# Kernel tuning notes

Hardware: AMD Instinct MI355X
Metric: run time of the kernel (lower is better)

## Reference

```python
import jax, jax.numpy as jnp
import numpy as np
import math

B, S, CIN, H, W = 8, 8, 64, 32, 32
COUT, K = 128, 3
PW = COUT * CIN * K * K  # 73728
P = PW + COUT            # 73856


def setup_inputs() -> dict:
    key = jax.random.key(0)
    ks = jax.random.split(key, 6)
    return {
        "x": jax.random.normal(ks[0], (B, S, CIN, H, W), dtype=jnp.float32),
        "e": jax.random.normal(ks[1], (S, P), dtype=jnp.float32),
        "mu_w": jax.random.normal(ks[2], (PW,), dtype=jnp.float32) * 0.02,
        "rho_w": jax.random.normal(ks[3], (PW,), dtype=jnp.float32) * 0.5,
        "mu_b": jax.random.normal(ks[4], (COUT,), dtype=jnp.float32) * 0.02,
        "rho_b": jax.random.normal(ks[5], (COUT,), dtype=jnp.float32) * 0.5,
    }


def _unit_log_mfg(v):
    # v: [s_n, D]; -log(2*pi)*D/2 - sum(v**2)/2  (scalar, matching torch code)
    two_pi = jnp.asarray(2.0 * math.pi, v.dtype)
    return -jnp.log(two_pi) * (v.shape[1] / 2.0) - jnp.sum(v * v) / 2.0


def reference(x, e, mu_w, rho_w, mu_b, rho_b):
    s_n = e.shape[0]
    cout = mu_b.shape[0]
    cin = x.shape[2]
    k = int(round(math.sqrt(mu_w.shape[0] / (cout * cin))))
    pw = mu_w.shape[0]

    sig_w = jax.nn.softplus(rho_w)  # log(1+exp(rho))
    sig_b = jax.nn.softplus(rho_b)
    w = mu_w[None, :] + sig_w[None, :] * e[:, :pw]          # [s_n, PW]
    b = mu_b[None, :] + sig_b[None, :] * e[:, pw:pw + cout]  # [s_n, COUT]

    entropy_q = jnp.sum(jnp.log(sig_w)) + jnp.sum(jnp.log(sig_b))
    cross_entropy_qp = _unit_log_mfg(w) + _unit_log_mfg(b)
    kl_qp = -entropy_q - cross_entropy_qp

    w5 = w.reshape(s_n, cout, cin, k, k)  # per-sample OIHW kernels

    # per-sample conv: vmap over the sample axis j; batch conv over data axis i
    def conv_one(xj, wj):  # xj [B,CIN,H,W], wj [COUT,CIN,K,K]
        return jax.lax.conv(xj, wj, (1, 1), 'VALID')

    out = jax.vmap(conv_one, in_axes=(1, 0), out_axes=1)(x, w5)  # [B,S,COUT,H',W']
    out = out + b[None, :, :, None, None]
    return out, kl_qp
```

## Files before the change

### kernel.cpp

```cpp
#include <hip/hip_runtime.h>
#include <hip/hip_bf16.h>
#include <math.h>

#define Bn    8
#define Sn    8
#define COUTc 128
#define PWc   73728
#define Pc    73856
#define WOc   30
#define NPIX  900
#define GPIX  7200
#define NSTEP 9
#define TILE  128
#define NT2   57

typedef __bf16 bf16;
typedef bf16  bf16x8 __attribute__((ext_vector_type(8)));
typedef float f32x16 __attribute__((ext_vector_type(16)));

__device__ __forceinline__ float softplus_f(float x) {
    return fmaxf(x, 0.f) + log1pf(expf(-fabsf(x)));
}

__device__ __forceinline__ unsigned int pack2(float a, float b) {
    unsigned short ua = __builtin_bit_cast(unsigned short, (bf16)a);
    unsigned short ub = __builtin_bit_cast(unsigned short, (bf16)b);
    return ((unsigned int)ub << 16) | (unsigned int)ua;
}

__device__ __forceinline__ void gl16(const void* g, void* l) {
    typedef __attribute__((address_space(1))) void gvoid;
    typedef __attribute__((address_space(3))) void lvoid;
    __builtin_amdgcn_global_load_lds((gvoid*)g, (lvoid*)l, 16, 0, 0);
}

__global__ __launch_bounds__(256) void prep_all(
        const float* __restrict__ xg, const float* __restrict__ e,
        const float* __restrict__ mu_w, const float* __restrict__ rho_w,
        const float* __restrict__ mu_b, const float* __restrict__ rho_b,
        bf16* __restrict__ xt, bf16* __restrict__ wimg,
        float* __restrict__ bq, float* __restrict__ slots) {
    const int bid = blockIdx.x;
    const int t   = threadIdx.x;

    if (bid < 512) {
        const int img  = bid >> 3;
        const int part = bid & 7;
        const int p    = part * 128 + (t >> 1);
        const int half = t & 1;
        const float* src = xg + ((size_t)img << 16) + (size_t)(half * 32) * 1024 + p;
        bf16*        dst = xt + ((size_t)img << 16) + (size_t)p * 64 + half * 32;
        #pragma unroll
        for (int o = 0; o < 4; ++o) {
            uint4 pk;
            pk.x = pack2(src[(o * 8 + 0) * 1024], src[(o * 8 + 1) * 1024]);
            pk.y = pack2(src[(o * 8 + 2) * 1024], src[(o * 8 + 3) * 1024]);
            pk.z = pack2(src[(o * 8 + 4) * 1024], src[(o * 8 + 5) * 1024]);
            pk.w = pack2(src[(o * 8 + 6) * 1024], src[(o * 8 + 7) * 1024]);
            *reinterpret_cast<uint4*>(dst + o * 8) = pk;
        }
        return;
    }

    float ls = 0.f, sq = 0.f;
    if (bid < 800) {
        const int rb    = bid - 512;
        const int r     = rb >> 5;
        const int chunk = rb & 31;
        const int idx   = chunk * 256 + t;
        const int co    = idx >> 6;
        const int ci    = idx & 63;
        const int p     = co * 576 + ci * 9 + r;
        float sig = softplus_f(rho_w[p]);
        ls = logf(sig);
        float mu = mu_w[p];
        const int dstp = (co << 6) + (((ci >> 3) ^ (co & 7)) << 3) + (ci & 7);
        #pragma unroll
        for (int s = 0; s < Sn; ++s) {
            float wv = fmaf(sig, e[s * Pc + p], mu);
            wimg[((s * NSTEP + r) << 13) + dstp] = (bf16)wv;
            sq += wv * wv;
        }
    } else {
        if (t < COUTc) {
            float sig = softplus_f(rho_b[t]);
            ls = logf(sig);
            float mu = mu_b[t];
            #pragma unroll
            for (int s = 0; s < Sn; ++s) {
                float bv = fmaf(sig, e[s * Pc + PWc + t], mu);
                bq[s * COUTc + t] = bv;
                sq += bv * bv;
            }
        }
    }

    #pragma unroll
    for (int off = 32; off > 0; off >>= 1) {
        ls += __shfl_down(ls, off);
        sq += __shfl_down(sq, off);
    }
    __shared__ float sls[4], ssq[4];
    const int lane = t & 63, wd = t >> 6;
    if (lane == 0) { sls[wd] = ls; ssq[wd] = sq; }
    __syncthreads();
    if (t == 0) {
        slots[2 * (bid - 512)]     = sls[0] + sls[1] + sls[2] + sls[3];
        slots[2 * (bid - 512) + 1] = ssq[0] + ssq[1] + ssq[2] + ssq[3];
    }
}

__global__ __launch_bounds__(256) void conv_mfma(
        const bf16* __restrict__ xt, const bf16* __restrict__ wimg,
        const float* __restrict__ bq, const float* __restrict__ slots,
        float* __restrict__ out, float* __restrict__ klout) {
    const int bid  = blockIdx.x;
    const int s    = bid & 7;
    const int tile = bid >> 3;
    const int t    = threadIdx.x;
    const int lane = t & 63;
    const int w    = t >> 6;
    const int wr   = w >> 1;
    const int wc   = w & 1;

    __shared__ bf16 Wbuf[2][8192];
    __shared__ bf16 Xbuf[2][8192];

    const char* wsrcL = (const char*)wimg + ((size_t)(s * NSTEP) << 14)
                      + (w << 12) + (lane << 4);

    const char *x0, *x1, *x2, *x3;
    #pragma unroll
    for (int q = 0; q < 4; ++q) {
        int pix = w * 32 + q * 8 + (lane >> 3);
        int g   = tile * TILE + pix;
        if (g >= GPIX) g = GPIX - 1;
        int b2 = g / NPIX;
        int rr = g - b2 * NPIX;
        int oy = rr / WOc;
        int ox = rr - oy * WOc;
        int m  = (lane & 7) ^ (pix & 7);
        const char* ptr = (const char*)xt
            + ((((size_t)(b2 * Sn + s) << 10) + oy * 32 + ox) << 7) + (m << 4);
        if (q == 0) x0 = ptr; else if (q == 1) x1 = ptr;
        else if (q == 2) x2 = ptr; else x3 = ptr;
    }

    f32x16 acc[2][2];
    #pragma unroll
    for (int i = 0; i < 2; ++i)
        #pragma unroll
        for (int j = 0; j < 2; ++j)
            #pragma unroll
            for (int k = 0; k < 16; ++k)
                acc[i][j][k] = 0.f;

    #define STAGE(stepc, b)                                                  \
    {                                                                        \
        const char* ws_ = wsrcL + ((stepc) << 14);                           \
        char* wl_ = (char*)(&Wbuf[(b)][0]) + (w << 12);                      \
        gl16(ws_,        wl_);                                               \
        gl16(ws_ + 1024, wl_ + 1024);                                        \
        gl16(ws_ + 2048, wl_ + 2048);                                        \
        gl16(ws_ + 3072, wl_ + 3072);                                        \
        const int roff_ = (((stepc) / 3) * 32 + ((stepc) % 3)) * 128;        \
        char* xl_ = (char*)(&Xbuf[(b)][0]) + (w << 12);                      \
        gl16(x0 + roff_, xl_);                                               \
        gl16(x1 + roff_, xl_ + 1024);                                        \
        gl16(x2 + roff_, xl_ + 2048);                                        \
        gl16(x3 + roff_, xl_ + 3072);                                        \
    }

    #define COMPUTE(b)                                                       \
    {                                                                        \
        const bf16* Wl_ = &Wbuf[(b)][0];                                     \
        const bf16* Xl_ = &Xbuf[(b)][0];                                     \
        _Pragma("unroll")                                                    \
        for (int kc = 0; kc < 4; ++kc) {                                     \
            const int oct_ = ((kc << 1) + (lane >> 5)) ^ (lane & 7);         \
            bf16x8 af0 = *reinterpret_cast<const bf16x8*>(                   \
                Wl_ + ((wr * 64 + (lane & 31)) << 6) + (oct_ << 3));         \
            bf16x8 af1 = *reinterpret_cast<const bf16x8*>(                   \
                Wl_ + ((wr * 64 + 32 + (lane & 31)) << 6) + (oct_ << 3));    \
            bf16x8 bf0 = *reinterpret_cast<const bf16x8*>(                   \
                Xl_ + ((wc * 64 + (lane & 31)) << 6) + (oct_ << 3));         \
            bf16x8 bf1 = *reinterpret_cast<const bf16x8*>(                   \
                Xl_ + ((wc * 64 + 32 + (lane & 31)) << 6) + (oct_ << 3));    \
            acc[0][0] = __builtin_amdgcn_mfma_f32_32x32x16_bf16(af0, bf0, acc[0][0], 0, 0, 0); \
            acc[0][1] = __builtin_amdgcn_mfma_f32_32x32x16_bf16(af0, bf1, acc[0][1], 0, 0, 0); \
            acc[1][0] = __builtin_amdgcn_mfma_f32_32x32x16_bf16(af1, bf0, acc[1][0], 0, 0, 0); \
            acc[1][1] = __builtin_amdgcn_mfma_f32_32x32x16_bf16(af1, bf1, acc[1][1], 0, 0, 0); \
        }                                                                    \
    }

    STAGE(0, 0);
    STAGE(1, 1);

    #define ITER(tt, b)                                                      \
        asm volatile("s_waitcnt vmcnt(8)" ::: "memory");                     \
        __builtin_amdgcn_s_barrier();                                        \
        __builtin_amdgcn_sched_barrier(0);                                   \
        COMPUTE(b);                                                          \
        __builtin_amdgcn_sched_barrier(0);                                   \
        __builtin_amdgcn_s_barrier();                                        \
        STAGE((tt) + 2, b);

    ITER(0, 0)
    ITER(1, 1)
    ITER(2, 0)
    ITER(3, 1)
    ITER(4, 0)
    ITER(5, 1)
    ITER(6, 0)
    asm volatile("s_waitcnt vmcnt(8)" ::: "memory");
    __builtin_amdgcn_s_barrier();
    __builtin_amdgcn_sched_barrier(0);
    COMPUTE(1);
    asm volatile("s_waitcnt vmcnt(0)" ::: "memory");
    __builtin_amdgcn_s_barrier();
    __builtin_amdgcn_sched_barrier(0);
    COMPUTE(0);

    #undef ITER
    #undef COMPUTE
    #undef STAGE

    const int colp = lane & 31;
    const int hi   = lane >> 5;
    #pragma unroll
    for (int ti = 0; ti < 2; ++ti) {
        float bs[16];
        #pragma unroll
        for (int reg = 0; reg < 16; ++reg) {
            int co = wr * 64 + ti * 32 + (reg & 3) + 8 * (reg >> 2) + 4 * hi;
            bs[reg] = bq[s * COUTc + co];
        }
        #pragma unroll
        for (int tj = 0; tj < 2; ++tj) {
            int gg = tile * TILE + wc * 64 + tj * 32 + colp;
            if (gg >= GPIX) continue;
            int b2 = gg / NPIX;
            int r2 = gg - b2 * NPIX;
            float* ob = out + (size_t)(b2 * Sn + s) * (COUTc * NPIX) + r2;
            #pragma unroll
            for (int reg = 0; reg < 16; ++reg) {
                int co = wr * 64 + ti * 32 + (reg & 3) + 8 * (reg >> 2) + 4 * hi;
                ob[co * NPIX] = acc[ti][tj][reg] + bs[reg];
            }
        }
    }

    if (bid == 0 && w == 0) {
        float ls = 0.f, sq = 0.f;
        for (int i = lane; i < 289; i += 64) {
            ls += slots[2 * i];
            sq += slots[2 * i + 1];
        }
        #pragma unroll
        for (int off = 32; off > 0; off >>= 1) {
            ls += __shfl_down(ls, off);
            sq += __shfl_down(sq, off);
        }
        if (lane == 0)
            *klout = -ls + 0.91893853320467274f * (float)Pc + 0.5f * sq;
    }
}

extern "C" void kernel_launch(void* const* d_in, const int* in_sizes, int n_in,
                              void* d_out, int out_size, void* d_ws, size_t ws_size,
                              hipStream_t stream) {
    const float* x     = (const float*)d_in[0];
    const float* e     = (const float*)d_in[1];
    const float* mu_w  = (const float*)d_in[2];
    const float* rho_w = (const float*)d_in[3];
    const float* mu_b  = (const float*)d_in[4];
    const float* rho_b = (const float*)d_in[5];
    float* out = (float*)d_out;

    bf16*  wimg  = (bf16*)d_ws;
    float* bq    = (float*)((char*)d_ws + 1179648);
    float* slots = (float*)((char*)d_ws + 1183744);
    bf16*  xt    = (bf16*)((char*)d_ws + 1187840);

    prep_all<<<dim3(801), dim3(256), 0, stream>>>(
        x, e, mu_w, rho_w, mu_b, rho_b, xt, wimg, bq, slots);

    conv_mfma<<<dim3(NT2 * Sn), dim3(256), 0, stream>>>(
        xt, wimg, bq, slots, out, out + (out_size - 1));
}
```

Before: 30.23 us.

## Vectorize prep loads, merge weight-tap blocks, restructure conv pipeline

The x transpose now reads float4 vectors per channel octet and writes four pixel rows per thread. Weight prep handles all nine taps per thread, so the launch shrinks from 801 to 545 blocks and each block reads e contiguously. The conv main loop changes from a 2-deep prefetch with vmcnt(8) to a one-stage-ahead pattern that waits for vmcnt(0) every iteration, which may expose more load latency. The KL slot reduction shrinks to a serial 33-entry loop on one thread.

```diff
diff --git a/kernel.cpp b/kernel.cpp
--- a/kernel.cpp
+++ b/kernel.cpp
@@ -16,6 +16,7 @@
 
 typedef __bf16 bf16;
 typedef bf16  bf16x8 __attribute__((ext_vector_type(8)));
+typedef float f32x4v __attribute__((ext_vector_type(4)));
 typedef float f32x16 __attribute__((ext_vector_type(16)));
 
 __device__ __forceinline__ float softplus_f(float x) {
@@ -44,42 +45,50 @@
     const int t   = threadIdx.x;
 
     if (bid < 512) {
-        const int img  = bid >> 3;
-        const int part = bid & 7;
-        const int p    = part * 128 + (t >> 1);
-        const int half = t & 1;
-        const float* src = xg + ((size_t)img << 16) + (size_t)(half * 32) * 1024 + p;
-        bf16*        dst = xt + ((size_t)img << 16) + (size_t)p * 64 + half * 32;
-        #pragma unroll
-        for (int o = 0; o < 4; ++o) {
+        const int img = bid >> 3;
+        const int oct = t & 7;
+        const int p0  = ((bid & 7) * 32 + (t >> 3)) * 4;
+        const float* src = xg + ((size_t)img << 16) + (size_t)(oct * 8) * 1024 + p0;
+        f32x4v v[8];
+        #pragma unroll
+        for (int j = 0; j < 8; ++j)
+            v[j] = *reinterpret_cast<const f32x4v*>(src + (size_t)j * 1024);
+        char* dstB = (char*)xt + (((size_t)(img << 10) + p0) << 7) + (oct << 4);
+        #pragma unroll
+        for (int i = 0; i < 4; ++i) {
             uint4 pk;
-            pk.x = pack2(src[(o * 8 + 0) * 1024], src[(o * 8 + 1) * 1024]);
-            pk.y = pack2(src[(o * 8 + 2) * 1024], src[(o * 8 + 3) * 1024]);
-            pk.z = pack2(src[(o * 8 + 4) * 1024], src[(o * 8 + 5) * 1024]);
-            pk.w = pack2(src[(o * 8 + 6) * 1024], src[(o * 8 + 7) * 1024]);
-            *reinterpret_cast<uint4*>(dst + o * 8) = pk;
+            pk.x = pack2(v[0][i], v[1][i]);
+            pk.y = pack2(v[2][i], v[3][i]);
+            pk.z = pack2(v[4][i], v[5][i]);
+            pk.w = pack2(v[6][i], v[7][i]);
+            *reinterpret_cast<uint4*>(dstB + (size_t)i * 128) = pk;
         }
         return;
     }
 
     float ls = 0.f, sq = 0.f;
-    if (bid < 800) {
-        const int rb    = bid - 512;
-        const int r     = rb >> 5;
-        const int chunk = rb & 31;
-        const int idx   = chunk * 256 + t;
-        const int co    = idx >> 6;
-        const int ci    = idx & 63;
-        const int p     = co * 576 + ci * 9 + r;
-        float sig = softplus_f(rho_w[p]);
-        ls = logf(sig);
-        float mu = mu_w[p];
+    if (bid < 544) {
+        const int gidx = (bid - 512) * 256 + t;
+        const int co   = gidx >> 6;
+        const int ci   = gidx & 63;
+        const int p0   = co * 576 + ci * 9;
+        float mu[9], sg[9];
+        #pragma unroll
+        for (int r = 0; r < 9; ++r) {
+            mu[r] = mu_w[p0 + r];
+            sg[r] = softplus_f(rho_w[p0 + r]);
+            ls   += logf(sg[r]);
+        }
         const int dstp = (co << 6) + (((ci >> 3) ^ (co & 7)) << 3) + (ci & 7);
         #pragma unroll
         for (int s = 0; s < Sn; ++s) {
-            float wv = fmaf(sig, e[s * Pc + p], mu);
-            wimg[((s * NSTEP + r) << 13) + dstp] = (bf16)wv;
-            sq += wv * wv;
+            const float* es = e + s * Pc + p0;
+            #pragma unroll
+            for (int r = 0; r < 9; ++r) {
+                float wv = fmaf(sg[r], es[r], mu[r]);
+                wimg[((s * NSTEP + r) << 13) + dstp] = (bf16)wv;
+                sq += wv * wv;
+            }
         }
     } else {
         if (t < COUTc) {
@@ -135,10 +144,7 @@
         int pix = w * 32 + q * 8 + (lane >> 3);
         int g   = tile * TILE + pix;
         if (g >= GPIX) g = GPIX - 1;
-        int b2 = g / NPIX;
-        int rr = g - b2 * NPIX;
-        int oy = rr / WOc;
-        int ox = rr - oy * WOc;
+        int b2 = g / NPIX, rr = g - b2 * NPIX, oy = rr / WOc, ox = rr - oy * WOc;
         int m  = (lane & 7) ^ (pix & 7);
         const char* ptr = (const char*)xt
             + ((((size_t)(b2 * Sn + s) << 10) + oy * 32 + ox) << 7) + (m << 4);
@@ -194,31 +200,25 @@
     }
 
     STAGE(0, 0);
-    STAGE(1, 1);
-
-    #define ITER(tt, b)                                                      \
-        asm volatile("s_waitcnt vmcnt(8)" ::: "memory");                     \
-        __builtin_amdgcn_s_barrier();                                        \
-        __builtin_amdgcn_sched_barrier(0);                                   \
-        COMPUTE(b);                                                          \
-        __builtin_amdgcn_sched_barrier(0);                                   \
-        __builtin_amdgcn_s_barrier();                                        \
-        STAGE((tt) + 2, b);
-
-    ITER(0, 0)
-    ITER(1, 1)
-    ITER(2, 0)
-    ITER(3, 1)
-    ITER(4, 0)
-    ITER(5, 1)
-    ITER(6, 0)
-    asm volatile("s_waitcnt vmcnt(8)" ::: "memory");
-    __builtin_amdgcn_s_barrier();
-    __builtin_amdgcn_sched_barrier(0);
-    COMPUTE(1);
     asm volatile("s_waitcnt vmcnt(0)" ::: "memory");
     __builtin_amdgcn_s_barrier();
     __builtin_amdgcn_sched_barrier(0);
+
+    #define ITER(tt)                                                         \
+        STAGE((tt) + 1, ((tt) + 1) & 1);                                     \
+        COMPUTE((tt) & 1);                                                   \
+        asm volatile("s_waitcnt vmcnt(0)" ::: "memory");                     \
+        __builtin_amdgcn_s_barrier();                                        \
+        __builtin_amdgcn_sched_barrier(0);
+
+    ITER(0)
+    ITER(1)
+    ITER(2)
+    ITER(3)
+    ITER(4)
+    ITER(5)
+    ITER(6)
+    ITER(7)
     COMPUTE(0);
 
     #undef ITER
@@ -250,19 +250,13 @@
         }
     }
 
-    if (bid == 0 && w == 0) {
+    if (bid == 0 && t == 0) {
         float ls = 0.f, sq = 0.f;
-        for (int i = lane; i < 289; i += 64) {
-            ls += slots[2 * i];
-            sq += slots[2 * i + 1];
-        }
-        #pragma unroll
-        for (int off = 32; off > 0; off >>= 1) {
-            ls += __shfl_down(ls, off);
-            sq += __shfl_down(sq, off);
-        }
-        if (lane == 0)
-            *klout = -ls + 0.91893853320467274f * (float)Pc + 0.5f * sq;
+        for (int i2 = 0; i2 < 33; ++i2) {
+            ls += slots[2 * i2];
+            sq += slots[2 * i2 + 1];
+        }
+        *klout = -ls + 0.91893853320467274f * (float)Pc + 0.5f * sq;
     }
 }
 
@@ -282,7 +276,7 @@
     float* slots = (float*)((char*)d_ws + 1183744);
     bf16*  xt    = (bf16*)((char*)d_ws + 1187840);
 
-    prep_all<<<dim3(801), dim3(256), 0, stream>>>(
+    prep_all<<<dim3(545), dim3(256), 0, stream>>>(
         x, e, mu_w, rho_w, mu_b, rho_b, xt, wimg, bq, slots);
 
     conv_mfma<<<dim3(NT2 * Sn), dim3(256), 0, stream>>>(
```

Result: slower. 33.49 us (+10.8%).
